# Kernel optimization log

Hardware: AMD Instinct MI355X
Metric: run time of the kernel (lower is better)

The kernel has to match this reference:

```python
import jax, jax.numpy as jnp
import numpy as np

G, P, DEG = 1024, 75, 8            # graphs, nodes per graph, out-degree
N, E = G * P, G * P * DEG
KS, DIM = 5, 2
K = KS ** DIM                      # 25 spline weight matrices
VOX = 4                            # 2x2 voxel grid per graph (size=14 over [0,27.99])


def setup_inputs():
    key = jax.random.key(0)
    ks = jax.random.split(key, 14)
    x = jax.random.uniform(ks[0], (N, 1), dtype=jnp.float32)            # pixel intensities
    src = jnp.repeat(jnp.arange(N, dtype=jnp.int32), DEG)
    dst = (src // P) * P + jax.random.randint(ks[1], (E,), 0, P, dtype=jnp.int32)
    edge_index = jnp.stack([src, dst])                                   # [2,E], within-graph edges
    edge_attr = jax.random.uniform(ks[2], (E, DIM), dtype=jnp.float32)  # Cartesian pseudo-coords in [0,1]
    batch = jnp.repeat(jnp.arange(G, dtype=jnp.int32), P)
    pos = jax.random.uniform(ks[3], (N, DIM), dtype=jnp.float32) * 27.99

    def nrm(k, shape, fan_in):
        return jax.random.normal(k, shape, jnp.float32) / np.float32(np.sqrt(fan_in))

    W1 = nrm(ks[4], (K, 1, 32), 1.0)
    root1 = nrm(ks[5], (1, 32), 1.0)
    b1 = jnp.zeros((32,), jnp.float32)
    W2 = nrm(ks[6], (K, 32, 64), 32.0)
    root2 = nrm(ks[7], (32, 64), 32.0)
    b2 = jnp.zeros((64,), jnp.float32)
    W3 = nrm(ks[8], (K, 64, 64), 64.0)
    root3 = nrm(ks[9], (64, 64), 64.0)
    b3 = jnp.zeros((64,), jnp.float32)
    fc1_w = nrm(ks[10], (4 * 64, 128), 256.0)
    fc1_b = jnp.zeros((128,), jnp.float32)
    fc2_w = nrm(ks[11], (128, 10), 128.0)
    fc2_b = jnp.zeros((10,), jnp.float32)
    return dict(x=x, edge_index=edge_index, edge_attr=edge_attr, batch=batch, pos=pos,
                W1=W1, root1=root1, b1=b1, W2=W2, root2=root2, b2=b2,
                W3=W3, root3=root3, b3=b3,
                fc1_w=fc1_w, fc1_b=fc1_b, fc2_w=fc2_w, fc2_b=fc2_b)


def spline_basis(u):
    """Degree-1 open B-spline basis, dim=2, kernel_size=5. u:[E,2] in [0,1].
    Returns basis [E,4] and flat weight indices [E,4]."""
    p = u * (KS - 1)
    lo = jnp.clip(jnp.floor(p), 0.0, KS - 1)
    frac = p - lo
    lo_i = lo.astype(jnp.int32)
    hi_i = jnp.minimum(lo_i + 1, KS - 1)
    w0 = jnp.stack([1.0 - frac[:, 0], frac[:, 0]], 1)   # [E,2]
    w1 = jnp.stack([1.0 - frac[:, 1], frac[:, 1]], 1)
    i0 = jnp.stack([lo_i[:, 0], hi_i[:, 0]], 1)
    i1 = jnp.stack([lo_i[:, 1], hi_i[:, 1]], 1)
    basis = (w0[:, :, None] * w1[:, None, :]).reshape(-1, 4)      # [E,4]
    idx = (i0[:, :, None] + KS * i1[:, None, :]).reshape(-1, 4)   # [E,4]
    return basis, idx


def spline_conv(h, src, dst, basis, idx, W, root, bias):
    # per-node transform under all K kernel weights: [N,K,O]
    y = jnp.einsum('ni,kio->nko', h, W)
    O = W.shape[2]
    msg = jnp.zeros((src.shape[0], O), h.dtype)
    for s in range(4):  # 4 B-spline corner contributions (fixed small loop)
        msg = msg + basis[:, s:s + 1] * y[src, idx[:, s]]
    agg = jax.ops.segment_sum(msg, dst, num_segments=N)
    deg = jax.ops.segment_sum(jnp.ones((src.shape[0],), h.dtype), dst, num_segments=N)
    agg = agg / jnp.maximum(deg, 1.0)[:, None]          # aggr='mean'
    return agg + h @ root + bias


def reference(x, edge_index, edge_attr, batch, pos,
              W1, root1, b1, W2, root2, b2, W3, root3, b3,
              fc1_w, fc1_b, fc2_w, fc2_b):
    src, dst = edge_index[0], edge_index[1]
    basis, idx = spline_basis(edge_attr)
    h = jax.nn.elu(spline_conv(x, src, dst, basis, idx, W1, root1, b1))
    h = jax.nn.elu(spline_conv(h, src, dst, basis, idx, W2, root2, b2))
    h = jax.nn.elu(spline_conv(h, src, dst, basis, idx, W3, root3, b3))
    # voxel_grid(size=14, start=0, end=27.99) -> 2x2 grid per graph
    vox = jnp.clip((pos / 14.0).astype(jnp.int32), 0, 1)          # [N,2]
    cluster = batch * VOX + vox[:, 0] + 2 * vox[:, 1]
    pooled = jax.ops.segment_max(h, cluster, num_segments=G * VOX)
    pooled = jnp.where(jnp.isneginf(pooled), 0.0, pooled)         # empty voxels -> 0
    graph_x = pooled.reshape(G, VOX * 64)                          # [G, 256]
    graph_x = jax.nn.elu(graph_x @ fc1_w + fc1_b)                  # dropout: eval mode (identity)
    logits = graph_x @ fc2_w + fc2_b
    return jax.nn.log_softmax(logits, axis=1)
```

## Files before the change

kernel.cpp:

```cpp
#include <hip/hip_runtime.h>
#include <math.h>

#define NG 1024
#define NP 75
#define NE_G 600
#define E_TOT 614400
#define NK 25
#define NSEG 1875
#define SST 104
#define YTST 104
#define HST 72

typedef _Float16 half8 __attribute__((ext_vector_type(8)));
typedef float floatx4 __attribute__((ext_vector_type(4)));

#define WS_WT2 0
#define WS_WT3 51200
#define WS_R2T 153600
#define WS_R3T 155648

__device__ __forceinline__ float elu_f(float x) {
    return x > 0.f ? x : (expf(x) - 1.f);
}
__device__ __forceinline__ float h16f(unsigned short b) {
    union { unsigned short u; _Float16 h; } c; c.u = b; return (float)c.h;
}
__device__ __forceinline__ _Float16 bits16(unsigned short b) {
    union { unsigned short u; _Float16 h; } c; c.u = b; return c.h;
}
__device__ __forceinline__ unsigned short f16bits(float v) {
    union { _Float16 h; unsigned short u; } c; c.h = (_Float16)v; return c.u;
}

__global__ void __launch_bounds__(256) prep_weights(
    const float* __restrict__ W2, const float* __restrict__ root2,
    const float* __restrict__ W3, const float* __restrict__ root3,
    _Float16* __restrict__ ws)
{
    int i = blockIdx.x * 256 + threadIdx.x;
    int stride = gridDim.x * 256;
    for (int t = i; t < 25 * 64 * 32; t += stride) {
        int k = t >> 11, o = (t >> 5) & 63, ci = t & 31;
        ws[WS_WT2 + t] = (_Float16)W2[(k * 32 + ci) * 64 + o];
    }
    for (int t = i; t < 25 * 64 * 64; t += stride) {
        int k = t >> 12, o = (t >> 6) & 63, ci = t & 63;
        ws[WS_WT3 + t] = (_Float16)W3[(k * 64 + ci) * 64 + o];
    }
    for (int t = i; t < 64 * 32; t += stride) {
        int o = t >> 5, ci = t & 31;
        ws[WS_R2T + t] = (_Float16)root2[ci * 64 + o];
    }
    for (int t = i; t < 64 * 64; t += stride) {
        int o = t >> 6, ci = t & 63;
        ws[WS_R3T + t] = (_Float16)root3[ci * 64 + o];
    }
}

struct EdgeB { int dl; int kk[4]; unsigned short bas[4]; };
__device__ __forceinline__ EdgeB edge_basis(const float* __restrict__ attr,
                                            const int* __restrict__ eidx,
                                            int g, int e) {
    EdgeB r;
    int ge = g * NE_G + e;
    r.dl = eidx[E_TOT + ge] - g * NP;
    float p0 = attr[2 * ge + 0] * 4.f, p1 = attr[2 * ge + 1] * 4.f;
    float fl0 = fminf(fmaxf(floorf(p0), 0.f), 4.f);
    float fl1 = fminf(fmaxf(floorf(p1), 0.f), 4.f);
    float fr0 = p0 - fl0, fr1 = p1 - fl1;
    int i00 = (int)fl0, i10 = (int)fl1;
    int i01 = min(i00 + 1, 4), i11 = min(i10 + 1, 4);
    float w0a[2] = {1.f - fr0, fr0};
    float w1a[2] = {1.f - fr1, fr1};
    int i0a[2] = {i00, i01};
    int i1a[2] = {i10, i11};
    #pragma unroll
    for (int a = 0; a < 2; ++a)
        #pragma unroll
        for (int b = 0; b < 2; ++b) {
            int s = a * 2 + b;
            r.kk[s] = i0a[a] + 5 * i1a[b];
            r.bas[s] = f16bits(w0a[a] * w1a[b]);
        }
    return r;
}

template<int CIN>
__device__ __forceinline__ void conv_layer(
    const _Float16* __restrict__ Wt,
    const _Float16* __restrict__ rootT,
    const float* __restrict__ bias,
    _Float16* __restrict__ sb_S,
    _Float16* __restrict__ sb_yT,
    _Float16* __restrict__ sb_h,
    const unsigned* __restrict__ sb_list,
    const int* __restrict__ sb_koff,
    const float* __restrict__ sb_rdeg,
    int tid, int lane, int wid)
{
    const int m = lane & 15, q = (lane >> 4) & 3;
    const int o = wid * 16 + m;
    constexpr int KK = CIN / 32;

    half8 Ah[5][KK];
    #pragma unroll
    for (int mt = 0; mt < 5; ++mt)
        #pragma unroll
        for (int kk = 0; kk < KK; ++kk)
            Ah[mt][kk] = *(const half8*)&sb_h[(mt * 16 + m) * HST + kk * 32 + q * 8];

    floatx4 agg[5];
    #pragma unroll
    for (int mt = 0; mt < 5; ++mt) agg[mt] = (floatx4){0.f, 0.f, 0.f, 0.f};

    half8 Bc[KK], Bn[KK];
    #pragma unroll
    for (int kk = 0; kk < KK; ++kk)
        Bc[kk] = *(const half8*)&Wt[(0 * 64 + o) * CIN + kk * 32 + q * 8];

    for (int k = 0; k < NK; ++k) {
        const int jb = sb_koff[k] + tid, kend = sb_koff[k + 1];
        unsigned upre = (jb < kend) ? sb_list[jb] : 0u;
        const _Float16* nb = (k < NK - 1) ? &Wt[((k + 1) * 64 + o) * CIN]
                                          : &rootT[o * CIN];
        #pragma unroll
        for (int kk = 0; kk < KK; ++kk)
            Bn[kk] = *(const half8*)&nb[kk * 32 + q * 8];
        for (int t = tid; t < 80 * SST / 8; t += 256)
            ((floatx4*)sb_S)[t] = (floatx4){0.f, 0.f, 0.f, 0.f};
        #pragma unroll
        for (int mt = 0; mt < 5; ++mt) {
            floatx4 c = {0.f, 0.f, 0.f, 0.f};
            #pragma unroll
            for (int kk = 0; kk < KK; ++kk)
                c = __builtin_amdgcn_mfma_f32_16x16x32_f16(Ah[mt][kk], Bc[kk], c, 0, 0, 0);
            union { _Float16 h[4]; unsigned long long u64; } p;
            p.h[0] = (_Float16)c[0]; p.h[1] = (_Float16)c[1];
            p.h[2] = (_Float16)c[2]; p.h[3] = (_Float16)c[3];
            *(unsigned long long*)&sb_yT[o * YTST + mt * 16 + q * 4] = p.u64;
        }
        __syncthreads();
        {
            bool first = true;
            for (int j = jb; j < kend; j += 256) {
                unsigned u = first ? upre : sb_list[j];
                first = false;
                if (u >> 16)
                    sb_S[((u >> 7) & 127) * SST + (u & 127)] = bits16((unsigned short)(u >> 16));
            }
        }
        __syncthreads();
        {
            half8 B0 = *(const half8*)&sb_yT[o * YTST + 0 + q * 8];
            half8 B1 = *(const half8*)&sb_yT[o * YTST + 32 + q * 8];
            half8 B2 = *(const half8*)&sb_yT[o * YTST + 64 + q * 8];
            #pragma unroll
            for (int mt = 0; mt < 5; ++mt) {
                half8 a0 = *(const half8*)&sb_S[(mt * 16 + m) * SST + 0 + q * 8];
                half8 a1 = *(const half8*)&sb_S[(mt * 16 + m) * SST + 32 + q * 8];
                half8 a2 = *(const half8*)&sb_S[(mt * 16 + m) * SST + 64 + q * 8];
                floatx4 c = agg[mt];
                c = __builtin_amdgcn_mfma_f32_16x16x32_f16(a0, B0, c, 0, 0, 0);
                c = __builtin_amdgcn_mfma_f32_16x16x32_f16(a1, B1, c, 0, 0, 0);
                c = __builtin_amdgcn_mfma_f32_16x16x32_f16(a2, B2, c, 0, 0, 0);
                agg[mt] = c;
            }
        }
        #pragma unroll
        for (int kk = 0; kk < KK; ++kk) Bc[kk] = Bn[kk];
        __syncthreads();
    }

    float bo = bias[o];
    #pragma unroll
    for (int mt = 0; mt < 5; ++mt) {
        floatx4 c = {0.f, 0.f, 0.f, 0.f};
        #pragma unroll
        for (int kk = 0; kk < KK; ++kk)
            c = __builtin_amdgcn_mfma_f32_16x16x32_f16(Ah[mt][kk], Bc[kk], c, 0, 0, 0);
        #pragma unroll
        for (int r = 0; r < 4; ++r) {
            int n = mt * 16 + q * 4 + r;
            if (n < NP) {
                float v = agg[mt][r] * sb_rdeg[n] + c[r] + bo;
                sb_h[n * HST + o] = (_Float16)elu_f(v);
            }
        }
    }
    __syncthreads();
}

__global__ void __launch_bounds__(256, 3) mnist_spline_fused(
    const float* __restrict__ xg,
    const int* __restrict__ eidx,
    const float* __restrict__ attr,
    const float* __restrict__ pos,
    const float* __restrict__ W1, const float* __restrict__ root1, const float* __restrict__ b1,
    const float* __restrict__ b2, const float* __restrict__ b3,
    const float* __restrict__ fc1w, const float* __restrict__ fc1b,
    const float* __restrict__ fc2w, const float* __restrict__ fc2b,
    const _Float16* __restrict__ ws,
    float* __restrict__ out)
{
    const int g = blockIdx.x;
    const int tid = threadIdx.x;
    const int lane = tid & 63;
    const int wid = tid >> 6;

    __shared__ __align__(16) _Float16 sb_S[80 * SST];
    __shared__ __align__(16) _Float16 sb_yT[64 * YTST];
    __shared__ __align__(16) _Float16 sb_h[80 * HST];
    __shared__ __align__(16) unsigned sb_list[NE_G * 4];
    __shared__ int sb_koff[26];
    __shared__ float sb_x[80];
    __shared__ float sb_rdeg[80];
    __shared__ int sb_deg[80];
    __shared__ unsigned sb_vmask[12];
    __shared__ unsigned sb_wsum[8];

    unsigned* cnt32 = (unsigned*)sb_S;
    unsigned short* segoff = (unsigned short*)((char*)sb_S + 7552);
    _Float16* T1 = sb_S;
    _Float16* W1T = (_Float16*)((char*)sb_S + 11312);
    float* fc_part = (float*)sb_S;
    float* fc_gx = (float*)((char*)sb_S + 2048);
    float* fc_z1 = (float*)((char*)sb_S + 3072);

    for (int p = tid; p < 80; p += 256) sb_deg[p] = 0;
    for (int p = tid; p < NSEG; p += 256) cnt32[p] = 0u;
    for (int p = tid; p < 5 * HST / 2; p += 256)
        ((unsigned*)&sb_h[NP * HST])[p] = 0u;
    for (int p = tid; p < 64 * 12; p += 256) {
        int ch = p / 12, c = p % 12;
        ((unsigned*)sb_yT)[ch * (YTST / 2) + 40 + c] = 0u;
    }
    if (tid < 12) sb_vmask[tid] = 0u;
    for (int p = tid; p < 32 * 32; p += 256) {
        int k = p >> 5, o = p & 31;
        W1T[o * 32 + k] = (k < NK) ? (_Float16)W1[k * 32 + o] : (_Float16)0.f;
    }
    __syncthreads();

    for (int e = tid; e < NE_G; e += 256) {
        EdgeB eb = edge_basis(attr, eidx, g, e);
        atomicAdd(&sb_deg[eb.dl], 1);
        #pragma unroll
        for (int s = 0; s < 4; ++s)
            atomicAdd(&cnt32[eb.kk[s] * NP + eb.dl], 1u);
    }
    for (int n = tid; n < NP; n += 256) {
        int gn = g * NP + n;
        sb_x[n] = xg[gn];
        int v0 = min(max((int)(pos[2 * gn] * (1.f / 14.f)), 0), 1);
        int v1 = min(max((int)(pos[2 * gn + 1] * (1.f / 14.f)), 0), 1);
        int v = v0 + 2 * v1;
        atomicOr(&sb_vmask[v * 3 + (n >> 5)], 1u << (n & 31));
    }
    __syncthreads();

    {
        int base = tid * 8;
        unsigned c8[8], lsum = 0;
        #pragma unroll
        for (int i = 0; i < 8; ++i) {
            int idx = base + i;
            c8[i] = (idx < NSEG) ? cnt32[idx] : 0u;
            lsum += c8[i];
        }
        unsigned v = lsum;
        #pragma unroll
        for (int d = 1; d < 64; d <<= 1) {
            unsigned ov = __shfl_up(v, d);
            if (lane >= d) v += ov;
        }
        if (lane == 63) sb_wsum[wid] = v;
        __syncthreads();
        unsigned wpre = 0;
        for (int w2 = 0; w2 < wid; ++w2) wpre += sb_wsum[w2];
        unsigned run = wpre + v - lsum;
        #pragma unroll
        for (int i = 0; i < 8; ++i) {
            int idx = base + i;
            if (idx < NSEG + 1) segoff[idx] = (unsigned short)run;
            if (idx < NSEG) cnt32[idx] = run;
            run += c8[i];
        }
        if (tid < 80) sb_rdeg[tid] = (tid < NP) ? 1.f / fmaxf((float)sb_deg[tid], 1.f) : 0.f;
    }
    __syncthreads();

    for (int e = tid; e < NE_G; e += 256) {
        EdgeB eb = edge_basis(attr, eidx, g, e);
        int srcl = e >> 3;
        #pragma unroll
        for (int s = 0; s < 4; ++s) {
            unsigned p = atomicAdd(&cnt32[eb.kk[s] * NP + eb.dl], 1u);
            sb_list[p] = ((unsigned)eb.bas[s] << 16) | ((unsigned)eb.dl << 7) | (unsigned)srcl;
        }
    }
    if (tid < 26) sb_koff[tid] = segoff[min(tid * NP, NSEG)];
    __syncthreads();

    for (int s = tid; s < NSEG; s += 256) {
        int s0 = segoff[s], s1 = segoff[s + 1];
        float tsum = 0.f;
        for (int j = s0; j < s1; ++j) {
            unsigned u = sb_list[j];
            if (!(u >> 16)) continue;
            int src = u & 127;
            float bsum = h16f((unsigned short)(u >> 16));
            for (int j2 = j + 1; j2 < s1; ++j2) {
                unsigned u2 = sb_list[j2];
                if ((u2 & 127) == (unsigned)src && (u2 >> 16)) {
                    bsum += h16f((unsigned short)(u2 >> 16));
                    sb_list[j2] = u2 & 0xFFFFu;
                }
            }
            sb_list[j] = ((unsigned)f16bits(bsum) << 16) | (u & 0xFFFFu);
            tsum += bsum * sb_x[src];
        }
        int k = s / NP, d = s - k * NP;
        T1[d * 40 + k] = (_Float16)tsum;
    }
    for (int t = tid; t < NP * 15 + 5 * 40; t += 256) {
        int d, k;
        if (t < NP * 15) { d = t / 15; k = NK + t % 15; }
        else { int t2 = t - NP * 15; d = NP + t2 / 40; k = t2 % 40; }
        T1[d * 40 + k] = (_Float16)0.f;
    }
    __syncthreads();

    if (wid < 2) {
        const int m = lane & 15, q = (lane >> 4) & 3;
        const int o = wid * 16 + m;
        half8 Bw = *(const half8*)&W1T[o * 32 + q * 8];
        float rt = root1[o], bo = b1[o];
        #pragma unroll
        for (int mt = 0; mt < 5; ++mt) {
            half8 a = *(const half8*)&T1[(mt * 16 + m) * 40 + q * 8];
            floatx4 c = {0.f, 0.f, 0.f, 0.f};
            c = __builtin_amdgcn_mfma_f32_16x16x32_f16(a, Bw, c, 0, 0, 0);
            #pragma unroll
            for (int r = 0; r < 4; ++r) {
                int n = mt * 16 + q * 4 + r;
                if (n < NP) {
                    float v = c[r] * sb_rdeg[n] + sb_x[n] * rt + bo;
                    sb_h[n * HST + o] = (_Float16)elu_f(v);
                }
            }
        }
    }
    __syncthreads();

    conv_layer<32>(ws + WS_WT2, ws + WS_R2T, b2, sb_S, sb_yT, sb_h,
                   sb_list, sb_koff, sb_rdeg, tid, lane, wid);
    conv_layer<64>(ws + WS_WT3, ws + WS_R3T, b3, sb_S, sb_yT, sb_h,
                   sb_list, sb_koff, sb_rdeg, tid, lane, wid);

    {
        int v = wid, o = lane;
        float mval = -INFINITY;
        #pragma unroll 25
        for (int n = 0; n < NP; ++n) {
            float val = (float)sb_h[n * HST + o];
            bool sel = (sb_vmask[v * 3 + (n >> 5)] >> (n & 31)) & 1;
            mval = sel ? fmaxf(mval, val) : mval;
        }
        fc_gx[v * 64 + o] = (mval == -INFINITY) ? 0.f : mval;
    }
    __syncthreads();

    {
        float acc0 = 0.f, acc1 = 0.f;
        #pragma unroll 8
        for (int i = 0; i < 64; ++i) {
            int ii = wid * 64 + i;
            float xv = fc_gx[ii];
            acc0 += xv * fc1w[ii * 128 + lane];
            acc1 += xv * fc1w[ii * 128 + 64 + lane];
        }
        fc_part[wid * 128 + lane] = acc0;
        fc_part[wid * 128 + 64 + lane] = acc1;
    }
    __syncthreads();
    if (tid < 128) {
        float v = fc_part[tid] + fc_part[128 + tid] + fc_part[256 + tid] + fc_part[384 + tid]
                + fc1b[tid];
        fc_z1[tid] = elu_f(v);
    }
    __syncthreads();

    if (wid == 0) {
        int o = lane & 15, sg = lane >> 4;
        float acc = 0.f;
        if (o < 10) {
            #pragma unroll 8
            for (int i = sg * 32; i < sg * 32 + 32; ++i)
                acc += fc_z1[i] * fc2w[i * 10 + o];
        }
        acc += __shfl_xor(acc, 16);
        acc += __shfl_xor(acc, 32);
        float logit = (o < 10) ? (acc + fc2b[o]) : 0.f;
        float lv = (o < 10) ? logit : -INFINITY;
        float mx = lv;
        #pragma unroll
        for (int d = 1; d < 16; d <<= 1) mx = fmaxf(mx, __shfl_xor(mx, d));
        float ex = (o < 10) ? expf(logit - mx) : 0.f;
        float se = ex;
        #pragma unroll
        for (int d = 1; d < 16; d <<= 1) se += __shfl_xor(se, d);
        if (lane < 10) out[g * 10 + lane] = logit - mx - logf(se);
    }
}

extern "C" void kernel_launch(void* const* d_in, const int* in_sizes, int n_in,
                              void* d_out, int out_size, void* d_ws, size_t ws_size,
                              hipStream_t stream) {
    const float* xg    = (const float*)d_in[0];
    const int*   eidx  = (const int*)d_in[1];
    const float* attr  = (const float*)d_in[2];
    const float* pos   = (const float*)d_in[4];
    const float* W1    = (const float*)d_in[5];
    const float* root1 = (const float*)d_in[6];
    const float* b1    = (const float*)d_in[7];
    const float* W2    = (const float*)d_in[8];
    const float* root2 = (const float*)d_in[9];
    const float* b2    = (const float*)d_in[10];
    const float* W3    = (const float*)d_in[11];
    const float* root3 = (const float*)d_in[12];
    const float* b3    = (const float*)d_in[13];
    const float* fc1w  = (const float*)d_in[14];
    const float* fc1b  = (const float*)d_in[15];
    const float* fc2w  = (const float*)d_in[16];
    const float* fc2b  = (const float*)d_in[17];
    float* out = (float*)d_out;
    _Float16* ws = (_Float16*)d_ws;

    prep_weights<<<160, 256, 0, stream>>>(W2, root2, W3, root3, ws);
    mnist_spline_fused<<<NG, 256, 0, stream>>>(
        xg, eidx, attr, pos, W1, root1, b1, b2, b3,
        fc1w, fc1b, fc2w, fc2b, ws, out);
}
```

Measured before the change: 263.7 us.

## Alias node-feature buffer onto scratch LDS to fit four blocks per CU

Removes the separate sb_h shared array and aliases it onto the sb_S scratch region. W1T moves to sb_yT, and the FC scratch buffers are relocated. Extra barriers are added so the aliased regions are read into registers before they are overwritten, and the padding rows are re-zeroed after each layer. Launch bounds rise from 3 to 4 blocks per CU. The goal is to cut LDS per block so more graphs run concurrently, at the cost of added syncs and register pressure from the tighter launch bound.

```diff
diff --git a/kernel.cpp b/kernel.cpp
--- a/kernel.cpp
+++ b/kernel.cpp
@@ -108,6 +108,7 @@
         #pragma unroll
         for (int kk = 0; kk < KK; ++kk)
             Ah[mt][kk] = *(const half8*)&sb_h[(mt * 16 + m) * HST + kk * 32 + q * 8];
+    __syncthreads();
 
     floatx4 agg[5];
     #pragma unroll
@@ -187,10 +188,12 @@
             }
         }
     }
-    __syncthreads();
-}
-
-__global__ void __launch_bounds__(256, 3) mnist_spline_fused(
+    for (int p = tid; p < 5 * HST / 2; p += 256)
+        ((unsigned*)&sb_h[NP * HST])[p] = 0u;
+    __syncthreads();
+}
+
+__global__ void __launch_bounds__(256, 4) mnist_spline_fused(
     const float* __restrict__ xg,
     const int* __restrict__ eidx,
     const float* __restrict__ attr,
@@ -207,9 +210,8 @@
     const int lane = tid & 63;
     const int wid = tid >> 6;
 
-    __shared__ __align__(16) _Float16 sb_S[80 * SST];
+    __shared__ __align__(16) unsigned char sb_SU[80 * SST * 2];
     __shared__ __align__(16) _Float16 sb_yT[64 * YTST];
-    __shared__ __align__(16) _Float16 sb_h[80 * HST];
     __shared__ __align__(16) unsigned sb_list[NE_G * 4];
     __shared__ int sb_koff[26];
     __shared__ float sb_x[80];
@@ -218,13 +220,15 @@
     __shared__ unsigned sb_vmask[12];
     __shared__ unsigned sb_wsum[8];
 
-    unsigned* cnt32 = (unsigned*)sb_S;
-    unsigned short* segoff = (unsigned short*)((char*)sb_S + 7552);
-    _Float16* T1 = sb_S;
-    _Float16* W1T = (_Float16*)((char*)sb_S + 11312);
-    float* fc_part = (float*)sb_S;
-    float* fc_gx = (float*)((char*)sb_S + 2048);
-    float* fc_z1 = (float*)((char*)sb_S + 3072);
+    _Float16* sb_S = (_Float16*)sb_SU;
+    _Float16* sb_h = (_Float16*)sb_SU;
+    unsigned* cnt32 = (unsigned*)sb_SU;
+    unsigned short* segoff = (unsigned short*)(sb_SU + 11520);
+    _Float16* T1 = (_Float16*)sb_SU;
+    _Float16* W1T = (_Float16*)sb_yT;
+    float* fc_gx = (float*)(sb_SU + 11776);
+    float* fc_part = (float*)(sb_SU + 12800);
+    float* fc_z1 = (float*)(sb_SU + 14848);
 
     for (int p = tid; p < 80; p += 256) sb_deg[p] = 0;
     for (int p = tid; p < NSEG; p += 256) cnt32[p] = 0u;
@@ -235,11 +239,11 @@
         ((unsigned*)sb_yT)[ch * (YTST / 2) + 40 + c] = 0u;
     }
     if (tid < 12) sb_vmask[tid] = 0u;
+    __syncthreads();
     for (int p = tid; p < 32 * 32; p += 256) {
         int k = p >> 5, o = p & 31;
         W1T[o * 32 + k] = (k < NK) ? (_Float16)W1[k * 32 + o] : (_Float16)0.f;
     }
-    __syncthreads();
 
     for (int e = tid; e < NE_G; e += 256) {
         EdgeB eb = edge_basis(attr, eidx, g, e);
@@ -330,24 +334,32 @@
     }
     __syncthreads();
 
-    if (wid < 2) {
+    {
+        floatx4 l1c[5];
         const int m = lane & 15, q = (lane >> 4) & 3;
         const int o = wid * 16 + m;
-        half8 Bw = *(const half8*)&W1T[o * 32 + q * 8];
-        float rt = root1[o], bo = b1[o];
-        #pragma unroll
-        for (int mt = 0; mt < 5; ++mt) {
-            half8 a = *(const half8*)&T1[(mt * 16 + m) * 40 + q * 8];
-            floatx4 c = {0.f, 0.f, 0.f, 0.f};
-            c = __builtin_amdgcn_mfma_f32_16x16x32_f16(a, Bw, c, 0, 0, 0);
+        if (wid < 2) {
+            half8 Bw = *(const half8*)&W1T[o * 32 + q * 8];
             #pragma unroll
-            for (int r = 0; r < 4; ++r) {
-                int n = mt * 16 + q * 4 + r;
-                if (n < NP) {
-                    float v = c[r] * sb_rdeg[n] + sb_x[n] * rt + bo;
-                    sb_h[n * HST + o] = (_Float16)elu_f(v);
+            for (int mt = 0; mt < 5; ++mt) {
+                half8 a = *(const half8*)&T1[(mt * 16 + m) * 40 + q * 8];
+                floatx4 c = {0.f, 0.f, 0.f, 0.f};
+                l1c[mt] = __builtin_amdgcn_mfma_f32_16x16x32_f16(a, Bw, c, 0, 0, 0);
+            }
+        }
+        __syncthreads();
+        if (wid < 2) {
+            float rt = root1[o], bo = b1[o];
+            #pragma unroll
+            for (int mt = 0; mt < 5; ++mt)
+                #pragma unroll
+                for (int r = 0; r < 4; ++r) {
+                    int n = mt * 16 + q * 4 + r;
+                    if (n < NP) {
+                        float v = l1c[mt][r] * sb_rdeg[n] + sb_x[n] * rt + bo;
+                        sb_h[n * HST + o] = (_Float16)elu_f(v);
+                    }
                 }
-            }
         }
     }
     __syncthreads();
```

New measurement: 230.4 us. 12.6% less time.
